# Kernel tuning notes

Hardware: AMD Instinct MI355X
Metric: run time of the kernel (lower is better)

The kernel has to match this reference:

```python
import jax, jax.numpy as jnp
import numpy as np

WS = 7      # window_size
SS = 3      # shift_size
NH = 12     # num_heads
HD = 32     # head_dim (dim // num_heads)


def _ln(x, g, b, eps=1e-5):
    mu = jnp.mean(x, axis=-1, keepdims=True)
    var = jnp.mean((x - mu) ** 2, axis=-1, keepdims=True)
    return (x - mu) * jax.lax.rsqrt(var + eps) * g + b


def setup_inputs() -> dict:
    key = jax.random.key(0)
    ks = jax.random.split(key, 8)
    b, h, w, c = 32, 56, 56, 384
    hid = 4 * c
    s = 0.02
    return {
        "x": jax.random.normal(ks[0], (b, h * w, c), jnp.float32),
        "h": h,
        "w": w,
        "g1": jnp.ones((c,), jnp.float32),
        "b1": jnp.zeros((c,), jnp.float32),
        "wqkv": jax.random.normal(ks[1], (c, 3 * c), jnp.float32) * s,
        "bqkv": jnp.zeros((3 * c,), jnp.float32),
        "wproj": jax.random.normal(ks[2], (c, c), jnp.float32) * s,
        "bproj": jnp.zeros((c,), jnp.float32),
        "g2": jnp.ones((c,), jnp.float32),
        "b2": jnp.zeros((c,), jnp.float32),
        "wfc1": jax.random.normal(ks[3], (c, hid), jnp.float32) * s,
        "bfc1": jnp.zeros((hid,), jnp.float32),
        "wfc2": jax.random.normal(ks[4], (hid, c), jnp.float32) * s,
        "bfc2": jnp.zeros((c,), jnp.float32),
    }


def _swin_block(x, h, w, g1, b1, wqkv, bqkv, wproj, bproj, g2, b2, wfc1, bfc1, wfc2, bfc2):
    b, l, c = x.shape
    shortcut = x
    xn = _ln(x, g1, b1).reshape(b, h, w, c)
    pad_h = (WS - h % WS) % WS
    pad_w = (WS - w % WS) % WS
    if pad_h > 0 or pad_w > 0:
        xn = jnp.pad(xn, ((0, 0), (0, pad_h), (0, pad_w), (0, 0)))
    hp, wp = xn.shape[1], xn.shape[2]
    if SS > 0:
        xn = jnp.roll(xn, (-SS, -SS), axis=(1, 2))
    # window partition -> [b*nw, ws*ws, c]
    win = xn.reshape(b, hp // WS, WS, wp // WS, WS, c)
    win = win.transpose(0, 1, 3, 2, 4, 5).reshape(-1, WS * WS, c)
    # window attention
    bnw, n, _ = win.shape
    qkv = (win @ wqkv + bqkv).reshape(bnw, n, 3, NH, HD)
    q, k, v = qkv[:, :, 0], qkv[:, :, 1], qkv[:, :, 2]  # [bnw, n, nh, hd]
    scale = HD ** -0.5
    attn = jnp.einsum("bqhd,bkhd->bhqk", q, k) * scale
    attn = jax.nn.softmax(attn, axis=-1)
    out = jnp.einsum("bhqk,bkhd->bqhd", attn, v).reshape(bnw, n, c)
    out = out @ wproj + bproj
    # window reverse
    xo = out.reshape(b, hp // WS, wp // WS, WS, WS, c)
    xo = xo.transpose(0, 1, 3, 2, 4, 5).reshape(b, hp, wp, c)
    if SS > 0:
        xo = jnp.roll(xo, (SS, SS), axis=(1, 2))
    if pad_h > 0 or pad_w > 0:
        xo = xo[:, :h, :w, :]
    xo = xo.reshape(b, h * w, c)
    xo = shortcut + xo
    # MLP with residual
    y = _ln(xo, g2, b2)
    y = jax.nn.gelu(y @ wfc1 + bfc1, approximate=False) @ wfc2 + bfc2
    return xo + y


def reference(x, h, w, g1, b1, wqkv, bqkv, wproj, bproj, g2, b2, wfc1, bfc1, wfc2, bfc2):
    return _swin_block(x, h, w, g1, b1, wqkv, bqkv, wproj, bproj,
                       g2, b2, wfc1, bfc1, wfc2, bfc2)
```

## Files before the change

### kernel.cpp

```cpp
#include <hip/hip_runtime.h>
#include <math.h>


typedef float f32x4 __attribute__((ext_vector_type(4)));
typedef float f32x2 __attribute__((ext_vector_type(2)));
typedef __bf16 bf16x8 __attribute__((ext_vector_type(8)));
typedef short s16x8 __attribute__((ext_vector_type(8)));
typedef unsigned short u16x2 __attribute__((ext_vector_type(2)));

#define DEV static __device__ __forceinline__

DEV unsigned short f2bf(float f) {
  unsigned int u = __builtin_bit_cast(unsigned int, f);
  u += 0x7fffu + ((u >> 16) & 1u);
  return (unsigned short)(u >> 16);
}
DEV float bf2f(unsigned short h) {
  unsigned int u = ((unsigned int)h) << 16;
  return __builtin_bit_cast(float, u);
}
DEV void load_lds16(const void* g, void* l) {
  __builtin_amdgcn_global_load_lds(
      (const __attribute__((address_space(1))) unsigned int*)g,
      (__attribute__((address_space(3))) unsigned int*)l, 16, 0, 0);
}

DEV int win_src_row(int row) {
  int win = row / 49, t = row - win * 49;
  int bimg = win >> 6, wrem = win & 63;
  int wy = wrem >> 3, wx = wrem & 7;
  int ti = t / 7, tj = t - ti * 7;
  int hh = wy * 7 + ti, ww = wx * 7 + tj;
  int sh = hh + 3; if (sh >= 56) sh -= 56;
  int sw = ww + 3; if (sw >= 56) sw -= 56;
  return bimg * 3136 + sh * 56 + sw;
}

__global__ void wt_kernel(const float* __restrict__ w, unsigned short* __restrict__ wt,
                          int Kd, int Nd) {
  int idx = blockIdx.x * 256 + threadIdx.x;
  if (idx >= Kd * Nd) return;
  int n = idx / Kd, k = idx - n * Kd;
  wt[idx] = f2bf(w[(size_t)k * Nd + n]);
}

template <int GATHER>
__global__ __launch_bounds__(256) void ln_kernel(const float* __restrict__ x,
                                                 const float* __restrict__ g,
                                                 const float* __restrict__ bb,
                                                 unsigned short* __restrict__ out) {
  int row = blockIdx.x * 4 + (threadIdx.x >> 6);
  int lane = threadIdx.x & 63;
  int src = GATHER ? win_src_row(row) : row;
  const float* xr = x + (size_t)src * 384;
  f32x2 p0 = *(const f32x2*)(xr + lane * 2);
  f32x2 p1 = *(const f32x2*)(xr + 128 + lane * 2);
  f32x2 p2 = *(const f32x2*)(xr + 256 + lane * 2);
  float s = p0.x + p0.y + p1.x + p1.y + p2.x + p2.y;
  float s2 = p0.x * p0.x + p0.y * p0.y + p1.x * p1.x + p1.y * p1.y +
             p2.x * p2.x + p2.y * p2.y;
#pragma unroll
  for (int off = 32; off; off >>= 1) {
    s += __shfl_xor(s, off);
    s2 += __shfl_xor(s2, off);
  }
  float mu = s * (1.0f / 384.0f);
  float rs = rsqrtf(s2 * (1.0f / 384.0f) - mu * mu + 1e-5f);
  unsigned short* orow = out + (size_t)row * 384;
  int c = lane * 2;
  u16x2 o;
  o.x = f2bf((p0.x - mu) * rs * g[c] + bb[c]);
  o.y = f2bf((p0.y - mu) * rs * g[c + 1] + bb[c + 1]);
  *(u16x2*)(orow + c) = o;
  c += 128;
  o.x = f2bf((p1.x - mu) * rs * g[c] + bb[c]);
  o.y = f2bf((p1.y - mu) * rs * g[c + 1] + bb[c + 1]);
  *(u16x2*)(orow + c) = o;
  c += 128;
  o.x = f2bf((p2.x - mu) * rs * g[c] + bb[c]);
  o.y = f2bf((p2.y - mu) * rs * g[c + 1] + bb[c + 1]);
  *(u16x2*)(orow + c) = o;
}

template <int EPI>
__global__ __launch_bounds__(256) void gemm_bt(const unsigned short* __restrict__ A,
                                               const unsigned short* __restrict__ BT,
                                               const float* __restrict__ bias, int Kd,
                                               int nTilesN, void* __restrict__ out0,
                                               const float* __restrict__ res) {
  __shared__ __attribute__((aligned(16))) unsigned short As[2][128 * 32];
  __shared__ __attribute__((aligned(16))) unsigned short Bs[2][128 * 32];
  const int tid = threadIdx.x;
  const int wid = tid >> 6, lane = tid & 63;
  const int nwg = gridDim.x;
  const int swz = (blockIdx.x & 7) * (nwg >> 3) + (blockIdx.x >> 3);
  const int bm = swz / nTilesN, bn = swz - bm * nTilesN;
  const int wr = wid >> 1, wc = wid & 1;
  f32x4 acc[4][4] = {};
  const int c0 = wid * 2;
  const int srow = lane >> 2;
  const int scol = (lane & 3) << 3;
  const unsigned short* gA0 = A + (size_t)(bm * 128 + c0 * 16 + srow) * Kd + scol;
  const unsigned short* gB0 = BT + (size_t)(bn * 128 + c0 * 16 + srow) * Kd + scol;
  const size_t row16 = (size_t)16 * Kd;
  const int lOff = c0 * 512;
  const int frow = lane & 15, fk = (lane >> 4) << 3;
  const int paOff = (wr * 64 + frow) * 32 + fk;
  const int pbOff = (wc * 64 + frow) * 32 + fk;

  auto STAGE = [&](int b, int k0) {
    unsigned short* lA = As[b] + lOff;
    unsigned short* lB = Bs[b] + lOff;
    load_lds16(gA0 + k0, lA);
    load_lds16(gA0 + k0 + row16, lA + 512);
    load_lds16(gB0 + k0, lB);
    load_lds16(gB0 + k0 + row16, lB + 512);
  };

  const int nk = Kd >> 5;
  STAGE(0, 0);
  __syncthreads();
  for (int t = 0; t < nk; ++t) {
    const int b = t & 1;
    if (t + 1 < nk) STAGE(b ^ 1, (t + 1) << 5);
    const unsigned short* pa = As[b] + paOff;
    const unsigned short* pb = Bs[b] + pbOff;
    bf16x8 af[4], bfv[4];
#pragma unroll
    for (int m = 0; m < 4; m++) af[m] = *(const bf16x8*)(pa + m * 512);
#pragma unroll
    for (int n = 0; n < 4; n++) bfv[n] = *(const bf16x8*)(pb + n * 512);
#pragma unroll
    for (int m = 0; m < 4; m++)
#pragma unroll
      for (int n = 0; n < 4; n++)
        acc[m][n] = __builtin_amdgcn_mfma_f32_16x16x32_bf16(af[m], bfv[n],
                                                            acc[m][n], 0, 0, 0);
    __syncthreads();
  }
  const int rbase = bm * 128 + wr * 64 + ((lane >> 4) << 2);
  const int cbase = bn * 128 + wc * 64 + (lane & 15);
#pragma unroll
  for (int m = 0; m < 4; m++) {
#pragma unroll
    for (int j = 0; j < 4; j++) {
      const int r = rbase + m * 16 + j;
      if constexpr (EPI == 0) {
        unsigned short* Qb = (unsigned short*)out0;
        int win = r / 49, t = r - win * 49;
        size_t base = (size_t)win * 18816 + (size_t)t * 32;
#pragma unroll
        for (int n = 0; n < 4; n++) {
          int cc = cbase + n * 16;
          float v = acc[m][n][j] + bias[cc];
          int which = cc / 384;
          int rem = cc - which * 384;
          int head = rem >> 5, d = rem & 31;
          Qb[(size_t)which * 38535168 + base + (size_t)head * 1568 + d] = f2bf(v);
        }
      } else if constexpr (EPI == 1) {
        float* XO = (float*)out0;
        size_t srowo = (size_t)win_src_row(r) * 384;
#pragma unroll
        for (int n = 0; n < 4; n++) {
          int cc = cbase + n * 16;
          XO[srowo + cc] = acc[m][n][j] + bias[cc] + res[srowo + cc];
        }
      } else if constexpr (EPI == 2) {
        unsigned short* H1 = (unsigned short*)out0;
        size_t ro = (size_t)r * 1536;
#pragma unroll
        for (int n = 0; n < 4; n++) {
          int cc = cbase + n * 16;
          float u = acc[m][n][j] + bias[cc];
          H1[ro + cc] = f2bf(0.5f * u * (1.0f + erff(u * 0.70710678118654752f)));
        }
      } else {
        float* O = (float*)out0;
        size_t ro = (size_t)r * 384;
#pragma unroll
        for (int n = 0; n < 4; n++) {
          int cc = cbase + n * 16;
          O[ro + cc] = acc[m][n][j] + bias[cc] + res[ro + cc];
        }
      }
    }
  }
}

__global__ __launch_bounds__(256) void attn_mfma(const unsigned short* __restrict__ Q,
                                                 const unsigned short* __restrict__ Kb,
                                                 const unsigned short* __restrict__ V,
                                                 unsigned short* __restrict__ AO) {
  __shared__ __attribute__((aligned(16))) unsigned short L[4][7168];
  const int wid = threadIdx.x >> 6, lane = threadIdx.x & 63;
  const int blk = blockIdx.x * 4 + wid;
  const int win = blk / 12, head = blk - win * 12;
  unsigned short* Qs = L[wid];
  unsigned short* Ks = Qs + 2048;
  unsigned short* VT = Qs + 4096;
  unsigned short* Ps = Qs + 6144;
  const unsigned short* Qp = Q + (size_t)blk * 1568;
  const unsigned short* Kp = Kb + (size_t)blk * 1568;
  const unsigned short* Vp = V + (size_t)blk * 1568;
  for (int i = lane; i < 196; i += 64) {
    int row = i >> 2, c8 = (i & 3) << 3;
    *(s16x8*)(Qs + row * 32 + c8) = *(const s16x8*)(Qp + i * 8);
    *(s16x8*)(Ks + row * 32 + c8) = *(const s16x8*)(Kp + i * 8);
    s16x8 vv = *(const s16x8*)(Vp + i * 8);
#pragma unroll
    for (int u = 0; u < 8; u++) VT[(c8 + u) * 64 + row] = (unsigned short)vv[u];
  }
  if (lane < 60) {
    s16x8 z = {};
    *(s16x8*)(Qs + 1568 + lane * 8) = z;
    *(s16x8*)(Ks + 1568 + lane * 8) = z;
  }
  for (int i = lane; i < 480; i += 64) {
    int d = i / 15, k = 49 + (i - d * 15);
    VT[d * 64 + k] = 0;
  }
  __syncthreads();

  const int g = lane >> 4, qi = lane & 15;
  const float scale = 0.17677669529663689f;
  bf16x8 kf[4];
#pragma unroll
  for (int mt = 0; mt < 4; mt++)
    kf[mt] = *(const bf16x8*)(Ks + (mt * 16 + qi) * 32 + g * 8);

  for (int nt = 0; nt < 4; nt++) {
    bf16x8 qf = *(const bf16x8*)(Qs + (nt * 16 + qi) * 32 + g * 8);
    f32x4 st[4];
#pragma unroll
    for (int mt = 0; mt < 4; mt++) {
      f32x4 zz = {};
      st[mt] = __builtin_amdgcn_mfma_f32_16x16x32_bf16(kf[mt], qf, zz, 0, 0, 0);
    }
    float m = -1e30f;
#pragma unroll
    for (int mt = 0; mt < 3; mt++)
#pragma unroll
      for (int j = 0; j < 4; j++) m = fmaxf(m, st[mt][j]);
    if (g == 0) m = fmaxf(m, st[3][0]);
    m = fmaxf(m, __shfl_xor(m, 16));
    m = fmaxf(m, __shfl_xor(m, 32));
    m *= scale;
    float p[4][4];
    float sum = 0.f;
#pragma unroll
    for (int mt = 0; mt < 4; mt++)
#pragma unroll
      for (int j = 0; j < 4; j++) {
        int k = mt * 16 + g * 4 + j;
        float e = (k < 49) ? __expf(st[mt][j] * scale - m) : 0.f;
        p[mt][j] = e;
        sum += e;
      }
    sum += __shfl_xor(sum, 16);
    sum += __shfl_xor(sum, 32);
    float inv = 1.0f / sum;
#pragma unroll
    for (int mt = 0; mt < 4; mt++)
#pragma unroll
      for (int j = 0; j < 4; j += 2) {
        unsigned int pk = (unsigned int)f2bf(p[mt][j]) |
                          ((unsigned int)f2bf(p[mt][j + 1]) << 16);
        *(unsigned int*)(Ps + qi * 64 + mt * 16 + g * 4 + j) = pk;
      }
    __syncthreads();
    f32x4 acc0 = {}, acc1 = {};
#pragma unroll
    for (int kt = 0; kt < 2; kt++) {
      bf16x8 pa = *(const bf16x8*)(Ps + qi * 64 + kt * 32 + g * 8);
      bf16x8 vb0 = *(const bf16x8*)(VT + qi * 64 + kt * 32 + g * 8);
      bf16x8 vb1 = *(const bf16x8*)(VT + (16 + qi) * 64 + kt * 32 + g * 8);
      acc0 = __builtin_amdgcn_mfma_f32_16x16x32_bf16(pa, vb0, acc0, 0, 0, 0);
      acc1 = __builtin_amdgcn_mfma_f32_16x16x32_bf16(pa, vb1, acc1, 0, 0, 0);
    }
#pragma unroll
    for (int jr = 0; jr < 4; jr++) {
      int q2 = g * 4 + jr;
      int qg = nt * 16 + q2;
      float iv = __shfl(inv, q2);
      if (qg < 49) {
        unsigned short* op = AO + ((size_t)win * 49 + qg) * 384 + head * 32 + qi;
        op[0] = f2bf(acc0[jr] * iv);
        op[16] = f2bf(acc1[jr] * iv);
      }
    }
    __syncthreads();
  }
}

extern "C" void kernel_launch(void* const* d_in, const int* in_sizes, int n_in,
                              void* d_out, int out_size, void* d_ws, size_t ws_size,
                              hipStream_t stream) {
  (void)in_sizes; (void)n_in; (void)out_size; (void)ws_size;
  const float* x = (const float*)d_in[0];
  const float* g1 = (const float*)d_in[3];
  const float* b1 = (const float*)d_in[4];
  const float* wqkv = (const float*)d_in[5];
  const float* bqkv = (const float*)d_in[6];
  const float* wproj = (const float*)d_in[7];
  const float* bproj = (const float*)d_in[8];
  const float* g2 = (const float*)d_in[9];
  const float* b2 = (const float*)d_in[10];
  const float* wfc1 = (const float*)d_in[11];
  const float* bfc1 = (const float*)d_in[12];
  const float* wfc2 = (const float*)d_in[13];
  const float* bfc2 = (const float*)d_in[14];

  char* ws = (char*)d_ws;
  unsigned short* wqkvT = (unsigned short*)ws;
  unsigned short* wprojT = wqkvT + 442368;
  unsigned short* wfc1T = wprojT + 147456;
  unsigned short* wfc2T = wfc1T + 589824;
  unsigned short* XW = wfc2T + 589824;
  unsigned short* Qb = XW + 38535168;
  unsigned short* Kb = Qb + 38535168;
  unsigned short* Vb = Kb + 38535168;
  unsigned short* AOb = XW;
  unsigned short* XN2 = Qb;
  unsigned short* H1buf = Kb;
  float* XO = (float*)d_out;
  float* out = (float*)d_out;

  wt_kernel<<<1728, 256, 0, stream>>>(wqkv, wqkvT, 384, 1152);
  wt_kernel<<<576, 256, 0, stream>>>(wproj, wprojT, 384, 384);
  wt_kernel<<<2304, 256, 0, stream>>>(wfc1, wfc1T, 384, 1536);
  wt_kernel<<<2304, 256, 0, stream>>>(wfc2, wfc2T, 1536, 384);

  ln_kernel<1><<<25088, 256, 0, stream>>>(x, g1, b1, XW);
  gemm_bt<0><<<784 * 9, 256, 0, stream>>>(XW, wqkvT, bqkv, 384, 9, Qb, nullptr);
  attn_mfma<<<6144, 256, 0, stream>>>(Qb, Kb, Vb, AOb);
  gemm_bt<1><<<784 * 3, 256, 0, stream>>>(AOb, wprojT, bproj, 384, 3, XO, x);
  ln_kernel<0><<<25088, 256, 0, stream>>>(XO, g2, b2, XN2);
  for (int ch = 0; ch < 2; ch++) {
    const unsigned short* a2 = XN2 + (size_t)ch * 50176 * 384;
    float* o2 = out + (size_t)ch * 50176 * 384;
    gemm_bt<2><<<392 * 12, 256, 0, stream>>>(a2, wfc1T, bfc1, 384, 12, H1buf, nullptr);
    gemm_bt<3><<<392 * 3, 256, 0, stream>>>(H1buf, wfc2T, bfc2, 1536, 3, o2, o2);
  }
}
```

Measured before the change: 1.037 ms.

## Enlarge GEMM tiles to 256xBN with BK=64 and 512-thread blocks

Replaces the 128x128x32 bf16 GEMM with a templated 256-row kernel using BK=64, 8 waves, and a 256- or 128-wide N tile chosen per GEMM. Each wave now computes up to 64x64 or 128x64 outputs. The XCD swizzle is changed to handle grid sizes that are not a multiple of 8. The larger tiles are meant to raise arithmetic intensity and cut global/LDS traffic per MFMA. In exchange they use more LDS (up to 128KB for the BN=256 case) and more accumulator registers, which may limit occupancy and leave fewer blocks per GEMM.

```diff
diff --git a/kernel.cpp b/kernel.cpp
--- a/kernel.cpp
+++ b/kernel.cpp
@@ -82,66 +82,76 @@
   *(u16x2*)(orow + c) = o;
 }
 
-template <int EPI>
-__global__ __launch_bounds__(256) void gemm_bt(const unsigned short* __restrict__ A,
-                                               const unsigned short* __restrict__ BT,
-                                               const float* __restrict__ bias, int Kd,
-                                               int nTilesN, void* __restrict__ out0,
-                                               const float* __restrict__ res) {
-  __shared__ __attribute__((aligned(16))) unsigned short As[2][128 * 32];
-  __shared__ __attribute__((aligned(16))) unsigned short Bs[2][128 * 32];
+template <int EPI, int BN>
+__global__ __launch_bounds__(512, 2) void gemm256(const unsigned short* __restrict__ A,
+                                                  const unsigned short* __restrict__ BT,
+                                                  const float* __restrict__ bias, int Kd,
+                                                  int nTilesN, void* __restrict__ out0,
+                                                  const float* __restrict__ res) {
+  constexpr int BM = 256, BK = 64;
+  constexpr int WAVES_N = (BN == 256) ? 4 : 2;
+  constexpr int WAVES_M = 8 / WAVES_N;
+  constexpr int WM = BM / WAVES_M;
+  constexpr int M_REP = WM / 16;
+  constexpr int ACHUNK = BM / 64;
+  constexpr int BCHUNK = BN / 64;
+  __shared__ __attribute__((aligned(16))) unsigned short As[2][BM * BK];
+  __shared__ __attribute__((aligned(16))) unsigned short Bs[2][BN * BK];
   const int tid = threadIdx.x;
   const int wid = tid >> 6, lane = tid & 63;
   const int nwg = gridDim.x;
-  const int swz = (blockIdx.x & 7) * (nwg >> 3) + (blockIdx.x >> 3);
+  const int xcd = blockIdx.x & 7, loc = blockIdx.x >> 3;
+  const int q = nwg >> 3, rr = nwg & 7;
+  const int swz = (xcd < rr ? xcd * (q + 1) : rr * (q + 1) + (xcd - rr) * q) + loc;
   const int bm = swz / nTilesN, bn = swz - bm * nTilesN;
-  const int wr = wid >> 1, wc = wid & 1;
-  f32x4 acc[4][4] = {};
-  const int c0 = wid * 2;
-  const int srow = lane >> 2;
-  const int scol = (lane & 3) << 3;
-  const unsigned short* gA0 = A + (size_t)(bm * 128 + c0 * 16 + srow) * Kd + scol;
-  const unsigned short* gB0 = BT + (size_t)(bn * 128 + c0 * 16 + srow) * Kd + scol;
-  const size_t row16 = (size_t)16 * Kd;
-  const int lOff = c0 * 512;
+  const int wr = wid / WAVES_N, wc = wid % WAVES_N;
+  f32x4 acc[M_REP][4] = {};
+  const int arow = tid >> 3, acol = (tid & 7) << 3;
+  const unsigned short* gA0 = A + (size_t)(bm * BM + arow) * Kd + acol;
+  const unsigned short* gB0 = BT + (size_t)(bn * BN + arow) * Kd + acol;
+  const size_t rowstep = (size_t)64 * Kd;
   const int frow = lane & 15, fk = (lane >> 4) << 3;
-  const int paOff = (wr * 64 + frow) * 32 + fk;
-  const int pbOff = (wc * 64 + frow) * 32 + fk;
 
   auto STAGE = [&](int b, int k0) {
-    unsigned short* lA = As[b] + lOff;
-    unsigned short* lB = Bs[b] + lOff;
-    load_lds16(gA0 + k0, lA);
-    load_lds16(gA0 + k0 + row16, lA + 512);
-    load_lds16(gB0 + k0, lB);
-    load_lds16(gB0 + k0 + row16, lB + 512);
+    unsigned short* lA = &As[b][tid * 8];
+    unsigned short* lB = &Bs[b][tid * 8];
+#pragma unroll
+    for (int s = 0; s < ACHUNK; s++)
+      load_lds16(gA0 + k0 + s * rowstep, lA + s * 4096);
+#pragma unroll
+    for (int s = 0; s < BCHUNK; s++)
+      load_lds16(gB0 + k0 + s * rowstep, lB + s * 4096);
   };
 
-  const int nk = Kd >> 5;
+  const int nk = Kd >> 6;
   STAGE(0, 0);
   __syncthreads();
   for (int t = 0; t < nk; ++t) {
     const int b = t & 1;
-    if (t + 1 < nk) STAGE(b ^ 1, (t + 1) << 5);
-    const unsigned short* pa = As[b] + paOff;
-    const unsigned short* pb = Bs[b] + pbOff;
-    bf16x8 af[4], bfv[4];
-#pragma unroll
-    for (int m = 0; m < 4; m++) af[m] = *(const bf16x8*)(pa + m * 512);
-#pragma unroll
-    for (int n = 0; n < 4; n++) bfv[n] = *(const bf16x8*)(pb + n * 512);
-#pragma unroll
-    for (int m = 0; m < 4; m++)
+    if (t + 1 < nk) STAGE(b ^ 1, (t + 1) << 6);
+    const unsigned short* pa = &As[b][(wr * WM + frow) * BK + fk];
+    const unsigned short* pb = &Bs[b][(wc * 64 + frow) * BK + fk];
+#pragma unroll
+    for (int ks = 0; ks < 2; ks++) {
+      bf16x8 bfr[4];
 #pragma unroll
       for (int n = 0; n < 4; n++)
-        acc[m][n] = __builtin_amdgcn_mfma_f32_16x16x32_bf16(af[m], bfv[n],
-                                                            acc[m][n], 0, 0, 0);
+        bfr[n] = *(const bf16x8*)(pb + n * 16 * BK + ks * 32);
+#pragma unroll
+      for (int m = 0; m < M_REP; m++) {
+        bf16x8 af = *(const bf16x8*)(pa + m * 16 * BK + ks * 32);
+#pragma unroll
+        for (int n = 0; n < 4; n++)
+          acc[m][n] = __builtin_amdgcn_mfma_f32_16x16x32_bf16(af, bfr[n],
+                                                              acc[m][n], 0, 0, 0);
+      }
+    }
     __syncthreads();
   }
-  const int rbase = bm * 128 + wr * 64 + ((lane >> 4) << 2);
-  const int cbase = bn * 128 + wc * 64 + (lane & 15);
-#pragma unroll
-  for (int m = 0; m < 4; m++) {
+  const int rbase = bm * BM + wr * WM + ((lane >> 4) << 2);
+  const int cbase = bn * BN + wc * 64 + (lane & 15);
+#pragma unroll
+  for (int m = 0; m < M_REP; m++) {
 #pragma unroll
     for (int j = 0; j < 4; j++) {
       const int r = rbase + m * 16 + j;
@@ -332,14 +342,14 @@
   wt_kernel<<<2304, 256, 0, stream>>>(wfc2, wfc2T, 1536, 384);
 
   ln_kernel<1><<<25088, 256, 0, stream>>>(x, g1, b1, XW);
-  gemm_bt<0><<<784 * 9, 256, 0, stream>>>(XW, wqkvT, bqkv, 384, 9, Qb, nullptr);
+  gemm256<0, 128><<<392 * 9, 512, 0, stream>>>(XW, wqkvT, bqkv, 384, 9, Qb, nullptr);
   attn_mfma<<<6144, 256, 0, stream>>>(Qb, Kb, Vb, AOb);
-  gemm_bt<1><<<784 * 3, 256, 0, stream>>>(AOb, wprojT, bproj, 384, 3, XO, x);
+  gemm256<1, 128><<<392 * 3, 512, 0, stream>>>(AOb, wprojT, bproj, 384, 3, XO, x);
   ln_kernel<0><<<25088, 256, 0, stream>>>(XO, g2, b2, XN2);
   for (int ch = 0; ch < 2; ch++) {
     const unsigned short* a2 = XN2 + (size_t)ch * 50176 * 384;
     float* o2 = out + (size_t)ch * 50176 * 384;
-    gemm_bt<2><<<392 * 12, 256, 0, stream>>>(a2, wfc1T, bfc1, 384, 12, H1buf, nullptr);
-    gemm_bt<3><<<392 * 3, 256, 0, stream>>>(H1buf, wfc2T, bfc2, 1536, 3, o2, o2);
-  }
-}
+    gemm256<2, 256><<<196 * 6, 512, 0, stream>>>(a2, wfc1T, bfc1, 384, 6, H1buf, nullptr);
+    gemm256<3, 128><<<196 * 3, 512, 0, stream>>>(H1buf, wfc2T, bfc2, 1536, 3, o2, o2);
+  }
+}
```

New measurement: 1.173 ms. 13.0% more time.
